# Performance work log

Hardware: AMD Instinct MI355X
Metric: run time of the kernel (lower is better)

The kernel has to match this reference:

```python
import jax, jax.numpy as jnp
import numpy as np
import math
from jax import lax

B, NP1, M, D, H, L, DFF = 16, 65, 256, 512, 8, 3, 2048
EPS_PROJ = 0.01  # MartingaleProjectionLayer is built with epsilon=0.01
LN_EPS = 1e-5


def _pos_encoding(n, d):
    pos = np.arange(n, dtype=np.float32)[:, None]
    div = np.exp(np.arange(0, d, 2, dtype=np.float32) * (-math.log(10000.0) / d))
    pe = np.zeros((n, d), dtype=np.float32)
    pe[:, 0::2] = np.sin(pos * div)
    pe[:, 1::2] = np.cos(pos * div)
    return jnp.asarray(pe)


def setup_inputs() -> dict:
    key = jax.random.key(0)
    ks = jax.random.split(key, 32)
    s = 0.02
    marg = jax.random.uniform(ks[0], (B, NP1, M), jnp.float32)
    marg = marg / marg.sum(axis=-1, keepdims=True)  # proper distributions
    return {
        "marginals": marg,
        "x_grid": jnp.linspace(-3.0, 3.0, M, dtype=jnp.float32),
        "conv_w": jax.random.normal(ks[1], (128, 1, 5), jnp.float32) * s,
        "conv_b": jax.random.normal(ks[2], (128,), jnp.float32) * s,
        "fc_w": jax.random.normal(ks[3], (128, D), jnp.float32) * s,
        "fc_b": jax.random.normal(ks[4], (D,), jnp.float32) * s,
        "ln0_g": jnp.ones((D,), jnp.float32),
        "ln0_b": jnp.zeros((D,), jnp.float32),
        "pos_enc": _pos_encoding(NP1, D),
        "qkv_w": jax.random.normal(ks[5], (L, 3 * D, D), jnp.float32) * s,
        "qkv_b": jax.random.normal(ks[6], (L, 3 * D), jnp.float32) * s,
        "out_w": jax.random.normal(ks[7], (L, D, D), jnp.float32) * s,
        "out_b": jax.random.normal(ks[8], (L, D), jnp.float32) * s,
        "ln1_g": jnp.ones((L, D), jnp.float32),
        "ln1_b": jnp.zeros((L, D), jnp.float32),
        "ff1_w": jax.random.normal(ks[9], (L, DFF, D), jnp.float32) * s,
        "ff1_b": jax.random.normal(ks[10], (L, DFF), jnp.float32) * s,
        "ff2_w": jax.random.normal(ks[11], (L, D, DFF), jnp.float32) * s,
        "ff2_b": jax.random.normal(ks[12], (L, D), jnp.float32) * s,
        "ln2_g": jnp.ones((L, D), jnp.float32),
        "ln2_b": jnp.zeros((L, D), jnp.float32),
        "u_w": jax.random.normal(ks[13], (M, D), jnp.float32) * s,
        "u_b": jax.random.normal(ks[14], (M,), jnp.float32) * s,
        "h_w": jax.random.normal(ks[15], (M, D), jnp.float32) * s,
        "h_b": jax.random.normal(ks[16], (M,), jnp.float32) * s,
    }


def _ln(x, g, b):
    mu = x.mean(axis=-1, keepdims=True)
    var = ((x - mu) ** 2).mean(axis=-1, keepdims=True)
    return (x - mu) * lax.rsqrt(var + LN_EPS) * g + b


def _gelu(x):
    return jax.nn.gelu(x, approximate=False)  # torch default exact GELU


def reference(marginals, x_grid, conv_w, conv_b, fc_w, fc_b, ln0_g, ln0_b,
              pos_enc, qkv_w, qkv_b, out_w, out_b, ln1_g, ln1_b,
              ff1_w, ff1_b, ff2_w, ff2_b, ln2_g, ln2_b, u_w, u_b, h_w, h_b):
    b, np1, m = marginals.shape
    n = np1 - 1
    d = fc_w.shape[1]
    nh = H
    dh = d // nh

    # ---- marginal embedding: Conv1d(1,128,k=5,pad=2) -> mean over grid -> FC+LN+GELU
    x = marginals.reshape(b * np1, 1, m)
    y = lax.conv_general_dilated(x, conv_w, (1,), [(2, 2)],
                                 dimension_numbers=("NCH", "OIH", "NCH"))
    y = y + conv_b[None, :, None]          # (b*np1, 128, m)
    emb = y.mean(axis=2)                   # (b*np1, 128)
    emb = _gelu(_ln(emb @ fc_w + fc_b, ln0_g, ln0_b))
    xs = emb.reshape(b, np1, d) + pos_enc[None, :np1, :]

    # ---- post-norm transformer encoder (dropout off / eval mode)
    scale = 1.0 / math.sqrt(dh)
    for l in range(L):
        qkv = xs @ qkv_w[l].T + qkv_b[l]                        # (b, s, 3d)
        q, k, v = jnp.split(qkv, 3, axis=-1)
        q = q.reshape(b, np1, nh, dh).transpose(0, 2, 1, 3)
        k = k.reshape(b, np1, nh, dh).transpose(0, 2, 1, 3)
        v = v.reshape(b, np1, nh, dh).transpose(0, 2, 1, 3)
        att = jax.nn.softmax(jnp.einsum("bhqd,bhkd->bhqk", q, k) * scale, axis=-1)
        o = jnp.einsum("bhqk,bhkd->bhqd", att, v)
        o = o.transpose(0, 2, 1, 3).reshape(b, np1, d)
        o = o @ out_w[l].T + out_b[l]
        xs = _ln(xs + o, ln1_g[l], ln1_b[l])
        ff = _gelu(xs @ ff1_w[l].T + ff1_b[l]) @ ff2_w[l].T + ff2_b[l]
        xs = _ln(xs + ff, ln2_g[l], ln2_b[l])

    u_pot = xs @ u_w.T + u_b                                    # (b, np1, M)
    h_raw = xs[:, :n, :] @ h_w.T + h_b                          # (b, n, M)

    # ---- vectorized martingale projection over all N timesteps
    x_diff = x_grid[:, None] - x_grid[None, :]                  # (M, M)
    h_kernel = h_raw[..., None] * x_diff                        # (b, n, M, M)
    P = jax.nn.softmax(h_kernel / EPS_PROJ, axis=-1)
    expected_next = jnp.einsum("bnij,j->bni", P, x_grid)
    drift = expected_next - x_grid                              # (b, n, M)
    mu = marginals[:, :n, :]
    weight_drift = (mu * drift).sum(axis=-1, keepdims=True)
    correction = weight_drift / (mu.sum(axis=-1, keepdims=True) + 1e-8)
    h_pot = h_raw - correction
    return (u_pot, h_pot)
```

## Files before the change

kernel.cpp:

```cpp
#include <hip/hip_runtime.h>
#include <math.h>


#define BT   1040
#define NP1  65
#define Dm   512
#define MG   256

typedef short short8 __attribute__((ext_vector_type(8)));
typedef float f32x4  __attribute__((ext_vector_type(4)));
typedef unsigned short u16;

__device__ __forceinline__ u16 f2bf(float f) {
  unsigned int u = __float_as_uint(f);
  u += 0x7FFF + ((u >> 16) & 1);
  return (u16)(u >> 16);
}
__device__ __forceinline__ float bf2f(u16 v) {
  return __uint_as_float(((unsigned int)v) << 16);
}

__device__ __forceinline__ float gelu_exact(float x) {
  return 0.5f * x * (1.0f + erff(x * 0.70710678118654752f));
}

__device__ __forceinline__ void async16(const u16* g, u16* l) {
  __builtin_amdgcn_global_load_lds(
      (const __attribute__((address_space(1))) unsigned int*)g,
      (__attribute__((address_space(3))) unsigned int*)l, 16, 0, 0);
}

__device__ __forceinline__ float wred(float v) {
#pragma unroll
  for (int o = 32; o; o >>= 1) v += __shfl_xor(v, o, 64);
  return v;
}

__device__ __forceinline__ float block_reduce_sum(float v, float* s) {
#pragma unroll
  for (int off = 32; off; off >>= 1) v += __shfl_down(v, off, 64);
  int lane = threadIdx.x & 63, wid = threadIdx.x >> 6;
  __syncthreads();
  if (lane == 0) s[wid] = v;
  __syncthreads();
  return s[0] + s[1] + s[2] + s[3];
}

__device__ __forceinline__ float f_closed(float a) {
  const float tf = 2.3529411765f;
  float t = a * tf;
  float s = fabsf(t);
  float E;
  if (s < 1e-4f) {
    E = 127.5f - 5461.25f * t;
  } else {
    float u = s * 256.0f;
    float term2 = (u < 80.0f) ? 256.0f / expm1f(u) : 0.0f;
    float Epos = 1.0f / expm1f(s) - term2;
    E = (t > 0.0f) ? Epos : 255.0f - Epos;
  }
  return -3.0f + 0.0235294118f * E;
}

__global__ __launch_bounds__(256) void embed4_kernel(
    const float* __restrict__ marg, const float* __restrict__ conv_w,
    const float* __restrict__ conv_b, const float* __restrict__ fc_w,
    const float* __restrict__ fc_b, const float* __restrict__ g,
    const float* __restrict__ bb, const float* __restrict__ pos,
    float* __restrict__ xs, u16* __restrict__ xsb)
{
  __shared__ float es[4][128];
  __shared__ float sS[4];
  __shared__ float edge[4][4];
  __shared__ float red[4];
  const int t0 = blockIdx.x * 4, tid = threadIdx.x;
  const int lane = tid & 63, wave = tid >> 6;
  {
    float4 mv = *(const float4*)(marg + (size_t)(t0 + wave) * MG + lane * 4);
    float S = wred(mv.x + mv.y + mv.z + mv.w);
    if (lane == 0) sS[wave] = S;
  }
  if (tid < 16) {
    int k = tid >> 2, e = tid & 3;
    int idx = (e < 2) ? e : (e + 252);
    edge[k][e] = marg[(size_t)(t0 + k) * MG + idx];
  }
  __syncthreads();
  if (tid < 128) {
    int o = tid;
    float w0 = conv_w[o*5+0], w1 = conv_w[o*5+1], w2 = conv_w[o*5+2];
    float w3 = conv_w[o*5+3], w4 = conv_w[o*5+4], cb = conv_b[o];
#pragma unroll
    for (int k = 0; k < 4; ++k) {
      float S = sS[k];
      float x0 = edge[k][0], x1 = edge[k][1], x254 = edge[k][2], x255 = edge[k][3];
      es[k][o] = (w0*(S - x254 - x255) + w1*(S - x255) + w2*S
                + w3*(S - x0) + w4*(S - x0 - x1)) * (1.0f/256.0f) + cb;
    }
  }
  __syncthreads();
  float b0 = fc_b[tid], b1 = fc_b[tid + 256];
  float z[4][2];
#pragma unroll
  for (int k = 0; k < 4; ++k) { z[k][0] = b0; z[k][1] = b1; }
#pragma unroll 4
  for (int o = 0; o < 128; ++o) {
    float f0 = fc_w[(size_t)o*Dm + tid];
    float f1 = fc_w[(size_t)o*Dm + tid + 256];
#pragma unroll
    for (int k = 0; k < 4; ++k) {
      float e = es[k][o];
      z[k][0] += e * f0; z[k][1] += e * f1;
    }
  }
  float g0 = g[tid], g1 = g[tid+256], e0 = bb[tid], e1 = bb[tid+256];
#pragma unroll
  for (int k = 0; k < 4; ++k) {
    float mu = block_reduce_sum(z[k][0] + z[k][1], red) * (1.0f/512.0f);
    float d0 = z[k][0] - mu, d1 = z[k][1] - mu;
    float var = block_reduce_sum(d0*d0 + d1*d1, red) * (1.0f/512.0f);
    float inv = rsqrtf(var + 1e-5f);
    int t = t0 + k, p = t % NP1;
    float y0 = gelu_exact(d0*inv*g0 + e0) + pos[(size_t)p*Dm + tid];
    float y1 = gelu_exact(d1*inv*g1 + e1) + pos[(size_t)p*Dm + tid + 256];
    xs[(size_t)t*Dm + tid]        = y0;
    xs[(size_t)t*Dm + tid + 256]  = y1;
    xsb[(size_t)t*Dm + tid]       = f2bf(y0);
    xsb[(size_t)t*Dm + tid + 256] = f2bf(y1);
  }
}

template<int SPLITS, int MODE>
__global__ __launch_bounds__(256) void gemm_f32b(
    const u16* __restrict__ A, const float* __restrict__ Bw,
    const float* __restrict__ Bw2, const float* __restrict__ bias,
    float* __restrict__ Cf, u16* __restrict__ Cb, float* __restrict__ C2,
    const float* __restrict__ bias2, int Mrows, int N, int K)
{
  __shared__ u16 Asl[8*64*8];
  __shared__ u16 Bsl[8*64*8];
  const int tid = threadIdx.x;
  const int row0 = blockIdx.y * 64, col0 = blockIdx.x * 64;
  const int Ks = K / SPLITS, kbase = (int)blockIdx.z * Ks;
  const int lane = tid & 63, wave = tid >> 6;
  const int wm = (wave >> 1) * 32, wn = (wave & 1) * 32;
  const int l15 = lane & 15, q = lane >> 4;

  f32x4 acc[2][2];
  acc[0][0] = (f32x4){0,0,0,0}; acc[0][1] = (f32x4){0,0,0,0};
  acc[1][0] = (f32x4){0,0,0,0}; acc[1][1] = (f32x4){0,0,0,0};

  const int arow = min(row0 + lane, Mrows - 1);
  const int gb = col0 + lane;
  const float* bsrc = (MODE == 3 && gb >= 256)
                        ? Bw2 + (size_t)(gb - 256) * K
                        : Bw  + (size_t)gb * K;
  for (int k0 = kbase; k0 < kbase + Ks; k0 += 64) {
    __syncthreads();
#pragma unroll
    for (int i = 0; i < 2; ++i) {
      int c = wave * 2 + i;
      async16(A + (size_t)arow * K + k0 + c * 8,
              &Asl[(size_t)(c * 64) * 8 + lane * 8]);
      const float* bp = bsrc + k0 + c * 8;
      float4 f0 = *(const float4*)bp;
      float4 f1 = *(const float4*)(bp + 4);
      u16 p[8] = { f2bf(f0.x), f2bf(f0.y), f2bf(f0.z), f2bf(f0.w),
                   f2bf(f1.x), f2bf(f1.y), f2bf(f1.z), f2bf(f1.w) };
      *(short8*)&Bsl[(size_t)(c * 64 + lane) * 8] = *(short8*)p;
    }
    __syncthreads();
#pragma unroll
    for (int t = 0; t < 2; ++t) {
      int cc = t * 4 + q;
      short8 af[2], bf[2];
#pragma unroll
      for (int mi = 0; mi < 2; ++mi)
        af[mi] = *(short8*)&Asl[(size_t)(cc*64 + wm + mi*16 + l15) * 8];
#pragma unroll
      for (int ni = 0; ni < 2; ++ni)
        bf[ni] = *(short8*)&Bsl[(size_t)(cc*64 + wn + ni*16 + l15) * 8];
#pragma unroll
      for (int mi = 0; mi < 2; ++mi)
#pragma unroll
        for (int ni = 0; ni < 2; ++ni)
          acc[mi][ni] = __builtin_amdgcn_mfma_f32_16x16x32_bf16(
              af[mi], bf[ni], acc[mi][ni], 0, 0, 0);
    }
  }

  float* Cp = Cf;
  if (MODE == 2) Cp += (size_t)blockIdx.z * (size_t)Mrows * N;
#pragma unroll
  for (int mi = 0; mi < 2; ++mi) {
#pragma unroll
    for (int ni = 0; ni < 2; ++ni) {
      int col = col0 + wn + ni*16 + l15;
#pragma unroll
      for (int r = 0; r < 4; ++r) {
        int row = row0 + wm + mi*16 + q*4 + r;
        if (row < Mrows) {
          float v = acc[mi][ni][r];
          if (MODE == 0) {
            Cb[(size_t)row*N + col] = f2bf(v + bias[col]);
          } else if (MODE == 1) {
            Cb[(size_t)row*N + col] = f2bf(gelu_exact(v + bias[col]));
          } else if (MODE == 2) {
            Cp[(size_t)row*N + col] = v;
          } else {
            if (col < 256) Cf[(size_t)row*256 + col]         = v + bias[col];
            else           C2[(size_t)row*256 + (col - 256)] = v + bias2[col - 256];
          }
        }
      }
    }
  }
}

__global__ __launch_bounds__(256) void attn_kernel(
    const u16* __restrict__ qkvb, u16* __restrict__ obufb)
{
  __shared__ float qv[65][67];
  __shared__ float ks[65][67];
  __shared__ float ss[65][67];
  const int b = blockIdx.x >> 3, h = blockIdx.x & 7;
  const int tid = threadIdx.x;
  const u16* base = qkvb + (size_t)b * NP1 * 1536 + h * 64;
  for (int idx = tid; idx < NP1 * 16; idx += 256) {
    int t = idx >> 4, c = (idx & 15) << 2;
    const u16* p = base + (size_t)t * 1536 + c;
    ushort4 q4 = *(const ushort4*)(p);
    ushort4 k4 = *(const ushort4*)(p + 512);
    qv[t][c] = bf2f(q4.x); qv[t][c+1] = bf2f(q4.y);
    qv[t][c+2] = bf2f(q4.z); qv[t][c+3] = bf2f(q4.w);
    ks[t][c] = bf2f(k4.x); ks[t][c+1] = bf2f(k4.y);
    ks[t][c+2] = bf2f(k4.z); ks[t][c+3] = bf2f(k4.w);
  }
  __syncthreads();
#pragma unroll
  for (int it = 0; it < 2; ++it) {
    int tile = it * 256 + tid;
    if (tile < 289) {
      int ti = (tile / 17) * 4, tj = (tile % 17) * 4;
      const float* qr[4]; const float* kr[4];
#pragma unroll
      for (int i = 0; i < 4; ++i) { qr[i] = qv[min(ti + i, 64)]; kr[i] = ks[min(tj + i, 64)]; }
      float acc[4][4] = {};
      for (int d = 0; d < 64; ++d) {
        float a[4], bvv[4];
#pragma unroll
        for (int i = 0; i < 4; ++i) { a[i] = qr[i][d]; bvv[i] = kr[i][d]; }
#pragma unroll
        for (int i = 0; i < 4; ++i)
#pragma unroll
          for (int j = 0; j < 4; ++j) acc[i][j] += a[i] * bvv[j];
      }
#pragma unroll
      for (int i = 0; i < 4; ++i)
        if (ti + i < 65)
#pragma unroll
          for (int j = 0; j < 4; ++j)
            if (tj + j < 65) ss[ti + i][tj + j] = acc[i][j] * 0.125f;
    }
  }
  __syncthreads();
  for (int idx = tid; idx < NP1 * 16; idx += 256) {
    int t = idx >> 4, c = (idx & 15) << 2;
    ushort4 v4 = *(const ushort4*)(base + (size_t)t * 1536 + 1024 + c);
    qv[t][c] = bf2f(v4.x); qv[t][c+1] = bf2f(v4.y);
    qv[t][c+2] = bf2f(v4.z); qv[t][c+3] = bf2f(v4.w);
  }
  if (tid < 65) {
    float mx = -1e30f;
    for (int j = 0; j < 65; ++j) mx = fmaxf(mx, ss[tid][j]);
    float s = 0.0f;
    for (int j = 0; j < 65; ++j) { float e = expf(ss[tid][j] - mx); ss[tid][j] = e; s += e; }
    float inv = 1.0f / s;
    for (int j = 0; j < 65; ++j) ss[tid][j] *= inv;
  }
  __syncthreads();
#pragma unroll
  for (int it = 0; it < 2; ++it) {
    int tile = it * 256 + tid;
    if (tile < 272) {
      int ti = (tile >> 4) * 4, d0 = (tile & 15) * 4;
      const float* sr[4];
#pragma unroll
      for (int i = 0; i < 4; ++i) sr[i] = ss[min(ti + i, 64)];
      float acc[4][4] = {};
      for (int j = 0; j < 65; ++j) {
        float v0 = qv[j][d0], v1 = qv[j][d0+1], v2 = qv[j][d0+2], v3 = qv[j][d0+3];
#pragma unroll
        for (int i = 0; i < 4; ++i) {
          float s = sr[i][j];
          acc[i][0] += s * v0; acc[i][1] += s * v1;
          acc[i][2] += s * v2; acc[i][3] += s * v3;
        }
      }
#pragma unroll
      for (int i = 0; i < 4; ++i)
        if (ti + i < 65) {
          ushort4 o;
          o.x = f2bf(acc[i][0]); o.y = f2bf(acc[i][1]);
          o.z = f2bf(acc[i][2]); o.w = f2bf(acc[i][3]);
          *(ushort4*)(obufb + (size_t)(b * NP1 + ti + i) * Dm + h * 64 + d0) = o;
        }
    }
  }
}

template<int S>
__global__ __launch_bounds__(256) void add_ln4(
    float* __restrict__ xs, u16* __restrict__ xsb,
    const float* __restrict__ part, const float* __restrict__ bias,
    const float* __restrict__ g, const float* __restrict__ bb)
{
  const int lane = threadIdx.x & 63, wave = threadIdx.x >> 6;
  const int t = blockIdx.x * 4 + wave;
  const int c0 = lane * 8;
  float* xp = xs + (size_t)t * Dm;
  float v[8];
  {
    float4 a0 = *(const float4*)(xp + c0), a1 = *(const float4*)(xp + c0 + 4);
    float4 b0 = *(const float4*)(bias + c0), b1 = *(const float4*)(bias + c0 + 4);
    v[0]=a0.x+b0.x; v[1]=a0.y+b0.y; v[2]=a0.z+b0.z; v[3]=a0.w+b0.w;
    v[4]=a1.x+b1.x; v[5]=a1.y+b1.y; v[6]=a1.z+b1.z; v[7]=a1.w+b1.w;
  }
#pragma unroll
  for (int s = 0; s < S; ++s) {
    const float* pp = part + (size_t)s*BT*Dm + (size_t)t*Dm + c0;
    float4 q0 = *(const float4*)pp, q1 = *(const float4*)(pp + 4);
    v[0]+=q0.x; v[1]+=q0.y; v[2]+=q0.z; v[3]+=q0.w;
    v[4]+=q1.x; v[5]+=q1.y; v[6]+=q1.z; v[7]+=q1.w;
  }
  float s1 = 0.f;
#pragma unroll
  for (int j = 0; j < 8; ++j) s1 += v[j];
  float mu = wred(s1) * (1.0f/512.0f);
  float s2 = 0.f;
#pragma unroll
  for (int j = 0; j < 8; ++j) { float d = v[j]-mu; s2 += d*d; }
  float inv = rsqrtf(wred(s2) * (1.0f/512.0f) + 1e-5f);
  float4 g0 = *(const float4*)(g + c0), g1 = *(const float4*)(g + c0 + 4);
  float4 e0 = *(const float4*)(bb + c0), e1 = *(const float4*)(bb + c0 + 4);
  float gg[8] = {g0.x,g0.y,g0.z,g0.w,g1.x,g1.y,g1.z,g1.w};
  float ee[8] = {e0.x,e0.y,e0.z,e0.w,e1.x,e1.y,e1.z,e1.w};
  float y[8]; u16 yb[8];
#pragma unroll
  for (int j = 0; j < 8; ++j) { y[j] = (v[j]-mu)*inv*gg[j] + ee[j]; yb[j] = f2bf(y[j]); }
  *(float4*)(xp + c0)     = make_float4(y[0],y[1],y[2],y[3]);
  *(float4*)(xp + c0 + 4) = make_float4(y[4],y[5],y[6],y[7]);
  *(short8*)(xsb + (size_t)t*Dm + c0) = *(short8*)yb;
}

__global__ __launch_bounds__(256) void proj_closed(
    const float* __restrict__ hbuf, const float* __restrict__ marg,
    const float* __restrict__ xg, float* __restrict__ out_h)
{
  const int tid = threadIdx.x, lane = tid & 63, wave = tid >> 6;
  const int rr = blockIdx.x * 4 + wave;
  const int b = rr >> 6, n = rr & 63;
  const int row = b * NP1 + n;
  const int i0 = lane * 4;
  float4 a4 = *(const float4*)(hbuf + (size_t)row * MG + i0);
  float4 x4 = *(const float4*)(xg + i0);
  float4 m4 = *(const float4*)(marg + (size_t)row * MG + i0);
  float av[4] = {a4.x, a4.y, a4.z, a4.w};
  float xv[4] = {x4.x, x4.y, x4.z, x4.w};
  float uv[4] = {m4.x, m4.y, m4.z, m4.w};
  float wd = 0.f, ms = 0.f;
#pragma unroll
  for (int k = 0; k < 4; ++k) {
    float drift = f_closed(av[k]) - xv[k];
    wd += uv[k] * drift; ms += uv[k];
  }
  wd = wred(wd); ms = wred(ms);
  float corr = wd / (ms + 1e-8f);
  *(float4*)(out_h + ((size_t)(b * 64 + n)) * MG + i0) =
      make_float4(av[0]-corr, av[1]-corr, av[2]-corr, av[3]-corr);
}

extern "C" void kernel_launch(void* const* d_in, const int* in_sizes, int n_in,
                              void* d_out, int out_size, void* d_ws, size_t ws_size,
                              hipStream_t stream)
{
  const float* marg   = (const float*)d_in[0];
  const float* xg     = (const float*)d_in[1];
  const float* conv_w = (const float*)d_in[2];
  const float* conv_b = (const float*)d_in[3];
  const float* fc_w   = (const float*)d_in[4];
  const float* fc_b   = (const float*)d_in[5];
  const float* ln0_g  = (const float*)d_in[6];
  const float* ln0_b  = (const float*)d_in[7];
  const float* pos    = (const float*)d_in[8];
  const float* qkv_w  = (const float*)d_in[9];
  const float* qkv_b  = (const float*)d_in[10];
  const float* out_w  = (const float*)d_in[11];
  const float* out_b  = (const float*)d_in[12];
  const float* ln1_g  = (const float*)d_in[13];
  const float* ln1_b  = (const float*)d_in[14];
  const float* ff1_w  = (const float*)d_in[15];
  const float* ff1_b  = (const float*)d_in[16];
  const float* ff2_w  = (const float*)d_in[17];
  const float* ff2_b  = (const float*)d_in[18];
  const float* ln2_g  = (const float*)d_in[19];
  const float* ln2_b  = (const float*)d_in[20];
  const float* u_w    = (const float*)d_in[21];
  const float* u_b    = (const float*)d_in[22];
  const float* h_w    = (const float*)d_in[23];
  const float* h_b    = (const float*)d_in[24];
  float* out = (float*)d_out;

  float* ws = (float*)d_ws;
  float* xs      = ws;
  float* part    = ws + 532480;
  float* hbuf    = ws + 2662400;
  u16*   xsb     = (u16*)(ws + 2928640);
  u16*   obufb   = (u16*)(ws + 3194880);
  u16*   ffb     = (u16*)(ws + 3461120);
  u16*   qkvb    = (u16*)(ws + 4526080);

  embed4_kernel<<<260, 256, 0, stream>>>(marg, conv_w, conv_b, fc_w, fc_b,
                                         ln0_g, ln0_b, pos, xs, xsb);

  for (int l = 0; l < 3; ++l) {
    gemm_f32b<1,0><<<dim3(24, 17), 256, 0, stream>>>(
        xsb, qkv_w + (size_t)l*786432, nullptr, qkv_b + l*1536,
        nullptr, qkvb, nullptr, nullptr, BT, 1536, 512);
    attn_kernel<<<128, 256, 0, stream>>>(qkvb, obufb);
    gemm_f32b<2,2><<<dim3(8, 17, 2), 256, 0, stream>>>(
        obufb, out_w + (size_t)l*262144, nullptr, nullptr, part,
        nullptr, nullptr, nullptr, BT, 512, 512);
    add_ln4<2><<<260, 256, 0, stream>>>(xs, xsb, part, out_b + l*512,
                                        ln1_g + l*512, ln1_b + l*512);
    gemm_f32b<1,1><<<dim3(32, 17), 256, 0, stream>>>(
        xsb, ff1_w + (size_t)l*1048576, nullptr, ff1_b + l*2048, nullptr,
        ffb, nullptr, nullptr, BT, 2048, 512);
    gemm_f32b<4,2><<<dim3(8, 17, 4), 256, 0, stream>>>(
        ffb, ff2_w + (size_t)l*1048576, nullptr, nullptr, part,
        nullptr, nullptr, nullptr, BT, 512, 2048);
    add_ln4<4><<<260, 256, 0, stream>>>(xs, xsb, part, ff2_b + l*512,
                                        ln2_g + l*512, ln2_b + l*512);
  }

  gemm_f32b<1,3><<<dim3(8, 17), 256, 0, stream>>>(
      xsb, u_w, h_w, u_b, out, nullptr, hbuf, h_b, BT, 512, 512);
  proj_closed<<<256, 256, 0, stream>>>(hbuf, marg, xg, out + 1040*256);
}
```

Baseline: 459.9 us.

## Keep QKV in fp32 and parallelize attention softmax across wavefront lanes

The QKV projection now writes fp32 output instead of bf16, and the attention kernel loads fp32 Q/K/V directly, removing the bf16 rounding step. The softmax no longer runs one row per thread over 65 threads. Each wavefront now handles a row using shuffle reductions for max and sum. This doubles QKV write and read traffic in exchange for better precision and a more parallel softmax.

```diff
diff --git a/kernel.cpp b/kernel.cpp
--- a/kernel.cpp
+++ b/kernel.cpp
@@ -16,9 +16,6 @@
   u += 0x7FFF + ((u >> 16) & 1);
   return (u16)(u >> 16);
 }
-__device__ __forceinline__ float bf2f(u16 v) {
-  return __uint_as_float(((unsigned int)v) << 16);
-}
 
 __device__ __forceinline__ float gelu_exact(float x) {
   return 0.5f * x * (1.0f + erff(x * 0.70710678118654752f));
@@ -33,6 +30,11 @@
 __device__ __forceinline__ float wred(float v) {
 #pragma unroll
   for (int o = 32; o; o >>= 1) v += __shfl_xor(v, o, 64);
+  return v;
+}
+__device__ __forceinline__ float wredmax(float v) {
+#pragma unroll
+  for (int o = 32; o; o >>= 1) v = fmaxf(v, __shfl_xor(v, o, 64));
   return v;
 }
 
@@ -201,15 +203,15 @@
         int row = row0 + wm + mi*16 + q*4 + r;
         if (row < Mrows) {
           float v = acc[mi][ni][r];
-          if (MODE == 0) {
-            Cb[(size_t)row*N + col] = f2bf(v + bias[col]);
-          } else if (MODE == 1) {
+          if (MODE == 1) {
             Cb[(size_t)row*N + col] = f2bf(gelu_exact(v + bias[col]));
           } else if (MODE == 2) {
             Cp[(size_t)row*N + col] = v;
-          } else {
+          } else if (MODE == 3) {
             if (col < 256) Cf[(size_t)row*256 + col]         = v + bias[col];
             else           C2[(size_t)row*256 + (col - 256)] = v + bias2[col - 256];
+          } else {
+            Cf[(size_t)row*N + col] = v + bias[col];
           }
         }
       }
@@ -218,23 +220,21 @@
 }
 
 __global__ __launch_bounds__(256) void attn_kernel(
-    const u16* __restrict__ qkvb, u16* __restrict__ obufb)
+    const float* __restrict__ qkv, u16* __restrict__ obufb)
 {
   __shared__ float qv[65][67];
   __shared__ float ks[65][67];
   __shared__ float ss[65][67];
   const int b = blockIdx.x >> 3, h = blockIdx.x & 7;
-  const int tid = threadIdx.x;
-  const u16* base = qkvb + (size_t)b * NP1 * 1536 + h * 64;
+  const int tid = threadIdx.x, lane = tid & 63, wave = tid >> 6;
+  const float* base = qkv + (size_t)b * NP1 * 1536 + h * 64;
   for (int idx = tid; idx < NP1 * 16; idx += 256) {
     int t = idx >> 4, c = (idx & 15) << 2;
-    const u16* p = base + (size_t)t * 1536 + c;
-    ushort4 q4 = *(const ushort4*)(p);
-    ushort4 k4 = *(const ushort4*)(p + 512);
-    qv[t][c] = bf2f(q4.x); qv[t][c+1] = bf2f(q4.y);
-    qv[t][c+2] = bf2f(q4.z); qv[t][c+3] = bf2f(q4.w);
-    ks[t][c] = bf2f(k4.x); ks[t][c+1] = bf2f(k4.y);
-    ks[t][c+2] = bf2f(k4.z); ks[t][c+3] = bf2f(k4.w);
+    const float* p = base + (size_t)t * 1536 + c;
+    float4 q4 = *(const float4*)(p);
+    float4 k4 = *(const float4*)(p + 512);
+    qv[t][c] = q4.x; qv[t][c+1] = q4.y; qv[t][c+2] = q4.z; qv[t][c+3] = q4.w;
+    ks[t][c] = k4.x; ks[t][c+1] = k4.y; ks[t][c+2] = k4.z; ks[t][c+3] = k4.w;
   }
   __syncthreads();
 #pragma unroll
@@ -266,17 +266,18 @@
   __syncthreads();
   for (int idx = tid; idx < NP1 * 16; idx += 256) {
     int t = idx >> 4, c = (idx & 15) << 2;
-    ushort4 v4 = *(const ushort4*)(base + (size_t)t * 1536 + 1024 + c);
-    qv[t][c] = bf2f(v4.x); qv[t][c+1] = bf2f(v4.y);
-    qv[t][c+2] = bf2f(v4.z); qv[t][c+3] = bf2f(v4.w);
-  }
-  if (tid < 65) {
-    float mx = -1e30f;
-    for (int j = 0; j < 65; ++j) mx = fmaxf(mx, ss[tid][j]);
-    float s = 0.0f;
-    for (int j = 0; j < 65; ++j) { float e = expf(ss[tid][j] - mx); ss[tid][j] = e; s += e; }
-    float inv = 1.0f / s;
-    for (int j = 0; j < 65; ++j) ss[tid][j] *= inv;
+    float4 v4 = *(const float4*)(base + (size_t)t * 1536 + 1024 + c);
+    qv[t][c] = v4.x; qv[t][c+1] = v4.y; qv[t][c+2] = v4.z; qv[t][c+3] = v4.w;
+  }
+  for (int r = wave; r < NP1; r += 4) {
+    float v0 = ss[r][lane];
+    float v1 = (lane == 0) ? ss[r][64] : -1e30f;
+    float m = wredmax(fmaxf(v0, v1));
+    float e0 = expf(v0 - m);
+    float e1 = (lane == 0) ? expf(v1 - m) : 0.0f;
+    float inv = 1.0f / wred(e0 + e1);
+    ss[r][lane] = e0 * inv;
+    if (lane == 0) ss[r][64] = e1 * inv;
   }
   __syncthreads();
 #pragma unroll
@@ -413,21 +414,21 @@
 
   float* ws = (float*)d_ws;
   float* xs      = ws;
-  float* part    = ws + 532480;
-  float* hbuf    = ws + 2662400;
-  u16*   xsb     = (u16*)(ws + 2928640);
-  u16*   obufb   = (u16*)(ws + 3194880);
-  u16*   ffb     = (u16*)(ws + 3461120);
-  u16*   qkvb    = (u16*)(ws + 4526080);
+  float* qkvbuf  = ws + 532480;
+  float* part    = ws + 2129920;
+  float* hbuf    = ws + 4259840;
+  u16*   xsb     = (u16*)(ws + 4526080);
+  u16*   obufb   = (u16*)(ws + 4792320);
+  u16*   ffb     = (u16*)(ws + 5058560);
 
   embed4_kernel<<<260, 256, 0, stream>>>(marg, conv_w, conv_b, fc_w, fc_b,
                                          ln0_g, ln0_b, pos, xs, xsb);
 
   for (int l = 0; l < 3; ++l) {
-    gemm_f32b<1,0><<<dim3(24, 17), 256, 0, stream>>>(
+    gemm_f32b<1,4><<<dim3(24, 17), 256, 0, stream>>>(
         xsb, qkv_w + (size_t)l*786432, nullptr, qkv_b + l*1536,
-        nullptr, qkvb, nullptr, nullptr, BT, 1536, 512);
-    attn_kernel<<<128, 256, 0, stream>>>(qkvb, obufb);
+        qkvbuf, nullptr, nullptr, nullptr, BT, 1536, 512);
+    attn_kernel<<<128, 256, 0, stream>>>(qkvbuf, obufb);
     gemm_f32b<2,2><<<dim3(8, 17, 2), 256, 0, stream>>>(
         obufb, out_w + (size_t)l*262144, nullptr, nullptr, part,
         nullptr, nullptr, nullptr, BT, 512, 512);
```

Result: slower. 481.0 us (+4.6%).
